# Optimization experiments

Hardware: AMD Instinct MI355X
Metric: run time of the kernel (lower is better)

## Reference

```python
import jax, jax.numpy as jnp
import numpy as np

N_HIDDEN = 32
N_LATENT = 8
FEATS = 128


def _prelu(x, a):
    return jnp.where(x >= 0, x, a * x)


def _gru_cell(x, h, w_ih, w_hh, b_ih, b_hh):
    # PyTorch GRU gate order: r, z, n
    gi = w_ih @ x + b_ih            # (3H,)
    gh = w_hh @ h + b_hh            # (3H,)
    i_r, i_z, i_n = jnp.split(gi, 3)
    h_r, h_z, h_n = jnp.split(gh, 3)
    r = jax.nn.sigmoid(i_r + h_r)
    z = jax.nn.sigmoid(i_z + h_z)
    n = jnp.tanh(i_n + r * h_n)
    return (1.0 - z) * n + z * h


def setup_inputs() -> dict:
    key = jax.random.key(0)
    ks = jax.random.split(key, 32)
    H, L, F = N_HIDDEN, N_LATENT, FEATS
    s = 0.1
    inp = {
        "x": jax.random.normal(ks[0], (F,), dtype=jnp.float32),
        "hidden": jax.random.uniform(ks[1], (2, 1, H), dtype=jnp.float32),
        "eps": jax.random.normal(ks[2], (L,), dtype=jnp.float32),
        # GRU layer 0 (input = feats)
        "w_ih0": jax.random.normal(ks[3], (3 * H, F), dtype=jnp.float32) * s,
        "w_hh0": jax.random.normal(ks[4], (3 * H, H), dtype=jnp.float32) * s,
        "b_ih0": jax.random.normal(ks[5], (3 * H,), dtype=jnp.float32) * s,
        "b_hh0": jax.random.normal(ks[6], (3 * H,), dtype=jnp.float32) * s,
        # GRU layer 1 (input = hidden)
        "w_ih1": jax.random.normal(ks[7], (3 * H, H), dtype=jnp.float32) * s,
        "w_hh1": jax.random.normal(ks[8], (3 * H, H), dtype=jnp.float32) * s,
        "b_ih1": jax.random.normal(ks[9], (3 * H,), dtype=jnp.float32) * s,
        "b_hh1": jax.random.normal(ks[10], (3 * H,), dtype=jnp.float32) * s,
        # encoder
        "enc_w1": jax.random.normal(ks[11], (H, H), dtype=jnp.float32) * s,
        "enc_b1": jax.random.normal(ks[12], (H,), dtype=jnp.float32) * s,
        "enc_a1": jnp.float32(0.25),
        "enc_w2": jax.random.normal(ks[13], (H, H), dtype=jnp.float32) * s,
        "enc_b2": jax.random.normal(ks[14], (H,), dtype=jnp.float32) * s,
        "enc_a2": jnp.float32(0.25),
        "enc_w3": jax.random.normal(ks[15], (2 * L, H), dtype=jnp.float32) * s,
        "enc_b3": jax.random.normal(ks[16], (2 * L,), dtype=jnp.float32) * s,
        # decoder
        "dec_w1": jax.random.normal(ks[17], (H, L), dtype=jnp.float32) * s,
        "dec_b1": jax.random.normal(ks[18], (H,), dtype=jnp.float32) * s,
        "dec_a1": jnp.float32(0.25),
        "dec_w2": jax.random.normal(ks[19], (H, H), dtype=jnp.float32) * s,
        "dec_b2": jax.random.normal(ks[20], (H,), dtype=jnp.float32) * s,
        "dec_a2": jnp.float32(0.25),
        "dec_w3": jax.random.normal(ks[21], (F, H), dtype=jnp.float32) * s,
        "dec_b3": jax.random.normal(ks[22], (F,), dtype=jnp.float32) * s,
    }
    return inp


def reference(x, hidden, eps,
              w_ih0, w_hh0, b_ih0, b_hh0,
              w_ih1, w_hh1, b_ih1, b_hh1,
              enc_w1, enc_b1, enc_a1, enc_w2, enc_b2, enc_a2, enc_w3, enc_b3,
              dec_w1, dec_b1, dec_a1, dec_w2, dec_b2, dec_a2, dec_w3, dec_b3):
    # single timestep, batch 1: treat everything as vectors
    h0 = _gru_cell(x, hidden[0, 0], w_ih0, w_hh0, b_ih0, b_hh0)   # (32,)
    h1 = _gru_cell(h0, hidden[1, 0], w_ih1, w_hh1, b_ih1, b_hh1)  # (32,)
    out = h1  # top-layer GRU output

    e = _prelu(enc_w1 @ out + enc_b1, enc_a1)
    e = _prelu(enc_w2 @ e + enc_b2, enc_a2)
    encoded = enc_w3 @ e + enc_b3                                  # (16,)
    mu, logvar = encoded[:N_LATENT], encoded[N_LATENT:]
    std = jnp.exp(0.5 * logvar)
    z = mu + eps * std

    d = _prelu(dec_w1 @ z + dec_b1, dec_a1)
    d = _prelu(dec_w2 @ d + dec_b2, dec_a2)
    decoded = jax.nn.sigmoid(dec_w3 @ d + dec_b3)                  # (feats,)

    hidden_new = jnp.stack([h0, h1])[:, None, :]                   # (2,1,32)
    return decoded, mu, logvar, hidden_new
```

## Files before the change

kernel.cpp:

```cpp
#include <hip/hip_runtime.h>
#include <math.h>

#define NH 32
#define NL 8
#define NF 128

__device__ __forceinline__ float dot_v4(const float* __restrict__ w,
                                        const float* __restrict__ s, int n4) {
    const float4* w4 = (const float4*)w;
    const float4* s4 = (const float4*)s;
    float acc = 0.f;
#pragma unroll 8
    for (int i = 0; i < n4; ++i) {
        float4 a = w4[i];
        float4 b = s4[i];
        acc = fmaf(a.x, b.x, acc);
        acc = fmaf(a.y, b.y, acc);
        acc = fmaf(a.z, b.z, acc);
        acc = fmaf(a.w, b.w, acc);
    }
    return acc;
}

__device__ __forceinline__ float sigmoidf_(float x) {
    return 1.0f / (1.0f + __expf(-x));
}

__device__ __forceinline__ float preluf_(float x, float a) {
    return x >= 0.0f ? x : a * x;
}

__global__ void __launch_bounds__(128)
omni_anomaly_kernel(const float* __restrict__ x,
                    const float* __restrict__ hidden,
                    const float* __restrict__ eps,
                    const float* __restrict__ w_ih0, const float* __restrict__ w_hh0,
                    const float* __restrict__ b_ih0, const float* __restrict__ b_hh0,
                    const float* __restrict__ w_ih1, const float* __restrict__ w_hh1,
                    const float* __restrict__ b_ih1, const float* __restrict__ b_hh1,
                    const float* __restrict__ enc_w1, const float* __restrict__ enc_b1,
                    const float* __restrict__ enc_a1,
                    const float* __restrict__ enc_w2, const float* __restrict__ enc_b2,
                    const float* __restrict__ enc_a2,
                    const float* __restrict__ enc_w3, const float* __restrict__ enc_b3,
                    const float* __restrict__ dec_w1, const float* __restrict__ dec_b1,
                    const float* __restrict__ dec_a1,
                    const float* __restrict__ dec_w2, const float* __restrict__ dec_b2,
                    const float* __restrict__ dec_a2,
                    const float* __restrict__ dec_w3, const float* __restrict__ dec_b3,
                    float* __restrict__ out) {
    __shared__ __align__(16) float sx[NF];
    __shared__ __align__(16) float sh0[NH];
    __shared__ __align__(16) float sh1[NH];
    __shared__ __align__(16) float gi[3 * NH];
    __shared__ __align__(16) float gh[3 * NH];
    __shared__ __align__(16) float h0n[NH];
    __shared__ __align__(16) float h1n[NH];
    __shared__ __align__(16) float e_buf[NH];
    __shared__ __align__(16) float e2_buf[NH];
    __shared__ __align__(16) float z_buf[NL];
    __shared__ __align__(16) float d1_buf[NH];
    __shared__ __align__(16) float d2_buf[NH];

    const int tid = threadIdx.x;

    if (tid < NF) sx[tid] = x[tid];
    if (tid < NH) {
        sh0[tid] = hidden[tid];
        sh1[tid] = hidden[NH + tid];
    }
    __syncthreads();

    if (tid < 3 * NH) {
        gi[tid] = dot_v4(w_ih0 + tid * NF, sx, NF / 4) + b_ih0[tid];
        gh[tid] = dot_v4(w_hh0 + tid * NH, sh0, NH / 4) + b_hh0[tid];
    }
    __syncthreads();
    if (tid < NH) {
        float r = sigmoidf_(gi[tid] + gh[tid]);
        float z = sigmoidf_(gi[NH + tid] + gh[NH + tid]);
        float n = tanhf(gi[2 * NH + tid] + r * gh[2 * NH + tid]);
        float h = (1.0f - z) * n + z * sh0[tid];
        h0n[tid] = h;
        out[NF + 2 * NL + tid] = h;
    }
    __syncthreads();

    if (tid < 3 * NH) {
        gi[tid] = dot_v4(w_ih1 + tid * NH, h0n, NH / 4) + b_ih1[tid];
        gh[tid] = dot_v4(w_hh1 + tid * NH, sh1, NH / 4) + b_hh1[tid];
    }
    __syncthreads();
    if (tid < NH) {
        float r = sigmoidf_(gi[tid] + gh[tid]);
        float z = sigmoidf_(gi[NH + tid] + gh[NH + tid]);
        float n = tanhf(gi[2 * NH + tid] + r * gh[2 * NH + tid]);
        float h = (1.0f - z) * n + z * sh1[tid];
        h1n[tid] = h;
        out[NF + 2 * NL + NH + tid] = h;
    }
    __syncthreads();

    if (tid < NH) {
        float v = dot_v4(enc_w1 + tid * NH, h1n, NH / 4) + enc_b1[tid];
        e_buf[tid] = preluf_(v, enc_a1[0]);
    }
    __syncthreads();

    if (tid < NH) {
        float v = dot_v4(enc_w2 + tid * NH, e_buf, NH / 4) + enc_b2[tid];
        e2_buf[tid] = preluf_(v, enc_a2[0]);
    }
    __syncthreads();

    if (tid < 2 * NL) {
        float v = dot_v4(enc_w3 + tid * NH, e2_buf, NH / 4) + enc_b3[tid];
        out[NF + tid] = v;
        if (tid < NL) {
            float lv = dot_v4(enc_w3 + (NL + tid) * NH, e2_buf, NH / 4) + enc_b3[NL + tid];
            float std_ = __expf(0.5f * lv);
            z_buf[tid] = v + eps[tid] * std_;
        }
    }
    __syncthreads();

    if (tid < NH) {
        float v = dot_v4(dec_w1 + tid * NL, z_buf, NL / 4) + dec_b1[tid];
        d1_buf[tid] = preluf_(v, dec_a1[0]);
    }
    __syncthreads();

    if (tid < NH) {
        float v = dot_v4(dec_w2 + tid * NH, d1_buf, NH / 4) + dec_b2[tid];
        d2_buf[tid] = preluf_(v, dec_a2[0]);
    }
    __syncthreads();

    if (tid < NF) {
        float v = dot_v4(dec_w3 + tid * NH, d2_buf, NH / 4) + dec_b3[tid];
        out[tid] = sigmoidf_(v);
    }
}

extern "C" void kernel_launch(void* const* d_in, const int* in_sizes, int n_in,
                              void* d_out, int out_size, void* d_ws, size_t ws_size,
                              hipStream_t stream) {
    const float* x      = (const float*)d_in[0];
    const float* hidden = (const float*)d_in[1];
    const float* eps    = (const float*)d_in[2];
    const float* w_ih0  = (const float*)d_in[3];
    const float* w_hh0  = (const float*)d_in[4];
    const float* b_ih0  = (const float*)d_in[5];
    const float* b_hh0  = (const float*)d_in[6];
    const float* w_ih1  = (const float*)d_in[7];
    const float* w_hh1  = (const float*)d_in[8];
    const float* b_ih1  = (const float*)d_in[9];
    const float* b_hh1  = (const float*)d_in[10];
    const float* enc_w1 = (const float*)d_in[11];
    const float* enc_b1 = (const float*)d_in[12];
    const float* enc_a1 = (const float*)d_in[13];
    const float* enc_w2 = (const float*)d_in[14];
    const float* enc_b2 = (const float*)d_in[15];
    const float* enc_a2 = (const float*)d_in[16];
    const float* enc_w3 = (const float*)d_in[17];
    const float* enc_b3 = (const float*)d_in[18];
    const float* dec_w1 = (const float*)d_in[19];
    const float* dec_b1 = (const float*)d_in[20];
    const float* dec_a1 = (const float*)d_in[21];
    const float* dec_w2 = (const float*)d_in[22];
    const float* dec_b2 = (const float*)d_in[23];
    const float* dec_a2 = (const float*)d_in[24];
    const float* dec_w3 = (const float*)d_in[25];
    const float* dec_b3 = (const float*)d_in[26];
    float* out = (float*)d_out;

    omni_anomaly_kernel<<<1, 128, 0, stream>>>(
        x, hidden, eps,
        w_ih0, w_hh0, b_ih0, b_hh0,
        w_ih1, w_hh1, b_ih1, b_hh1,
        enc_w1, enc_b1, enc_a1,
        enc_w2, enc_b2, enc_a2,
        enc_w3, enc_b3,
        dec_w1, dec_b1, dec_a1,
        dec_w2, dec_b2, dec_a2,
        dec_w3, dec_b3,
        out);
}
```

Measured before the change: 11.78 us.

## Run whole network in a single wavefront with wave barriers instead of block syncs

The kernel now launches one 64-thread wavefront and replaces __syncthreads with wave-level barriers, redistributing the GRU and decoder rows so each lane computes several outputs. It also fully unrolls the dot products with four independent accumulators, uses an exp-based tanh, and keeps the previous hidden state in registers. The aim is to cut block-wide barrier cost on a latency-bound serial chain. In exchange each lane does more sequential work, and correctness relies on LDS writes being visible within the wave after a wave barrier.

```diff
diff --git a/kernel.cpp b/kernel.cpp
--- a/kernel.cpp
+++ b/kernel.cpp
@@ -5,32 +5,38 @@
 #define NL 8
 #define NF 128
 
-__device__ __forceinline__ float dot_v4(const float* __restrict__ w,
-                                        const float* __restrict__ s, int n4) {
+#define WSYNC() __builtin_amdgcn_wave_barrier()
+
+template <int N4>
+__device__ __forceinline__ float dotN(const float* __restrict__ w,
+                                      const float* __restrict__ s) {
     const float4* w4 = (const float4*)w;
-    const float4* s4 = (const float4*)s;
-    float acc = 0.f;
-#pragma unroll 8
-    for (int i = 0; i < n4; ++i) {
+    float a0 = 0.f, a1 = 0.f, a2 = 0.f, a3 = 0.f;
+#pragma unroll
+    for (int i = 0; i < N4; ++i) {
         float4 a = w4[i];
-        float4 b = s4[i];
-        acc = fmaf(a.x, b.x, acc);
-        acc = fmaf(a.y, b.y, acc);
-        acc = fmaf(a.z, b.z, acc);
-        acc = fmaf(a.w, b.w, acc);
-    }
-    return acc;
+        a0 = fmaf(a.x, s[4 * i + 0], a0);
+        a1 = fmaf(a.y, s[4 * i + 1], a1);
+        a2 = fmaf(a.z, s[4 * i + 2], a2);
+        a3 = fmaf(a.w, s[4 * i + 3], a3);
+    }
+    return (a0 + a1) + (a2 + a3);
 }
 
 __device__ __forceinline__ float sigmoidf_(float x) {
     return 1.0f / (1.0f + __expf(-x));
 }
 
+__device__ __forceinline__ float tanhf_(float x) {
+    float e = __expf(2.0f * x);
+    return 1.0f - 2.0f / (e + 1.0f);
+}
+
 __device__ __forceinline__ float preluf_(float x, float a) {
     return x >= 0.0f ? x : a * x;
 }
 
-__global__ void __launch_bounds__(128)
+__global__ void __launch_bounds__(64)
 omni_anomaly_kernel(const float* __restrict__ x,
                     const float* __restrict__ hidden,
                     const float* __restrict__ eps,
@@ -52,93 +58,119 @@
     __shared__ __align__(16) float sx[NF];
     __shared__ __align__(16) float sh0[NH];
     __shared__ __align__(16) float sh1[NH];
-    __shared__ __align__(16) float gi[3 * NH];
-    __shared__ __align__(16) float gh[3 * NH];
+    __shared__ __align__(16) float gi0[3 * NH];
+    __shared__ __align__(16) float gh0[3 * NH];
+    __shared__ __align__(16) float gi1[3 * NH];
+    __shared__ __align__(16) float gh1[3 * NH];
     __shared__ __align__(16) float h0n[NH];
     __shared__ __align__(16) float h1n[NH];
-    __shared__ __align__(16) float e_buf[NH];
-    __shared__ __align__(16) float e2_buf[NH];
-    __shared__ __align__(16) float z_buf[NL];
-    __shared__ __align__(16) float d1_buf[NH];
-    __shared__ __align__(16) float d2_buf[NH];
-
-    const int tid = threadIdx.x;
-
-    if (tid < NF) sx[tid] = x[tid];
-    if (tid < NH) {
-        sh0[tid] = hidden[tid];
-        sh1[tid] = hidden[NH + tid];
-    }
-    __syncthreads();
-
-    if (tid < 3 * NH) {
-        gi[tid] = dot_v4(w_ih0 + tid * NF, sx, NF / 4) + b_ih0[tid];
-        gh[tid] = dot_v4(w_hh0 + tid * NH, sh0, NH / 4) + b_hh0[tid];
-    }
-    __syncthreads();
-    if (tid < NH) {
-        float r = sigmoidf_(gi[tid] + gh[tid]);
-        float z = sigmoidf_(gi[NH + tid] + gh[NH + tid]);
-        float n = tanhf(gi[2 * NH + tid] + r * gh[2 * NH + tid]);
-        float h = (1.0f - z) * n + z * sh0[tid];
-        h0n[tid] = h;
-        out[NF + 2 * NL + tid] = h;
-    }
-    __syncthreads();
-
-    if (tid < 3 * NH) {
-        gi[tid] = dot_v4(w_ih1 + tid * NH, h0n, NH / 4) + b_ih1[tid];
-        gh[tid] = dot_v4(w_hh1 + tid * NH, sh1, NH / 4) + b_hh1[tid];
-    }
-    __syncthreads();
-    if (tid < NH) {
-        float r = sigmoidf_(gi[tid] + gh[tid]);
-        float z = sigmoidf_(gi[NH + tid] + gh[NH + tid]);
-        float n = tanhf(gi[2 * NH + tid] + r * gh[2 * NH + tid]);
-        float h = (1.0f - z) * n + z * sh1[tid];
-        h1n[tid] = h;
-        out[NF + 2 * NL + NH + tid] = h;
-    }
-    __syncthreads();
-
-    if (tid < NH) {
-        float v = dot_v4(enc_w1 + tid * NH, h1n, NH / 4) + enc_b1[tid];
-        e_buf[tid] = preluf_(v, enc_a1[0]);
-    }
-    __syncthreads();
-
-    if (tid < NH) {
-        float v = dot_v4(enc_w2 + tid * NH, e_buf, NH / 4) + enc_b2[tid];
-        e2_buf[tid] = preluf_(v, enc_a2[0]);
-    }
-    __syncthreads();
-
-    if (tid < 2 * NL) {
-        float v = dot_v4(enc_w3 + tid * NH, e2_buf, NH / 4) + enc_b3[tid];
-        out[NF + tid] = v;
-        if (tid < NL) {
-            float lv = dot_v4(enc_w3 + (NL + tid) * NH, e2_buf, NH / 4) + enc_b3[NL + tid];
-            float std_ = __expf(0.5f * lv);
-            z_buf[tid] = v + eps[tid] * std_;
+    __shared__ __align__(16) float e1b[NH];
+    __shared__ __align__(16) float e2b[NH];
+    __shared__ __align__(16) float eo[2 * NL];
+    __shared__ __align__(16) float zb[NL];
+    __shared__ __align__(16) float d1b[NH];
+    __shared__ __align__(16) float d2b[NH];
+
+    const int t = threadIdx.x;
+
+    float h0reg = 0.f, h1reg = 0.f;
+    if (t < NF / 4) {
+        ((float4*)sx)[t] = ((const float4*)x)[t];
+    }
+    if (t < NH) {
+        h0reg = hidden[t];
+        h1reg = hidden[NH + t];
+        sh0[t] = h0reg;
+        sh1[t] = h1reg;
+    }
+    WSYNC();
+
+    gi0[t] = dotN<NF / 4>(w_ih0 + t * NF, sx) + b_ih0[t];
+    if (t < 32) {
+        int r = 64 + t;
+        gi0[r] = dotN<NF / 4>(w_ih0 + r * NF, sx) + b_ih0[r];
+    } else {
+        int r = 3 * (t - 32);
+        gh0[r + 0] = dotN<NH / 4>(w_hh0 + (r + 0) * NH, sh0) + b_hh0[r + 0];
+        gh0[r + 1] = dotN<NH / 4>(w_hh0 + (r + 1) * NH, sh0) + b_hh0[r + 1];
+        gh0[r + 2] = dotN<NH / 4>(w_hh0 + (r + 2) * NH, sh0) + b_hh0[r + 2];
+    }
+    WSYNC();
+
+    if (t < NH) {
+        float r = sigmoidf_(gi0[t] + gh0[t]);
+        float z = sigmoidf_(gi0[NH + t] + gh0[NH + t]);
+        float n = tanhf_(gi0[2 * NH + t] + r * gh0[2 * NH + t]);
+        float h = (1.0f - z) * n + z * h0reg;
+        h0n[t] = h;
+        out[NF + 2 * NL + t] = h;
+    }
+    WSYNC();
+
+#pragma unroll
+    for (int k = 0; k < 3; ++k) {
+        int d = t + 64 * k;
+        if (d < 3 * NH) {
+            gi1[d] = dotN<NH / 4>(w_ih1 + d * NH, h0n) + b_ih1[d];
+        } else {
+            int r = d - 3 * NH;
+            gh1[r] = dotN<NH / 4>(w_hh1 + r * NH, sh1) + b_hh1[r];
         }
     }
-    __syncthreads();
-
-    if (tid < NH) {
-        float v = dot_v4(dec_w1 + tid * NL, z_buf, NL / 4) + dec_b1[tid];
-        d1_buf[tid] = preluf_(v, dec_a1[0]);
-    }
-    __syncthreads();
-
-    if (tid < NH) {
-        float v = dot_v4(dec_w2 + tid * NH, d1_buf, NH / 4) + dec_b2[tid];
-        d2_buf[tid] = preluf_(v, dec_a2[0]);
-    }
-    __syncthreads();
-
-    if (tid < NF) {
-        float v = dot_v4(dec_w3 + tid * NH, d2_buf, NH / 4) + dec_b3[tid];
-        out[tid] = sigmoidf_(v);
+    WSYNC();
+
+    if (t < NH) {
+        float r = sigmoidf_(gi1[t] + gh1[t]);
+        float z = sigmoidf_(gi1[NH + t] + gh1[NH + t]);
+        float n = tanhf_(gi1[2 * NH + t] + r * gh1[2 * NH + t]);
+        float h = (1.0f - z) * n + z * h1reg;
+        h1n[t] = h;
+        out[NF + 2 * NL + NH + t] = h;
+    }
+    WSYNC();
+
+    if (t < NH) {
+        float v = dotN<NH / 4>(enc_w1 + t * NH, h1n) + enc_b1[t];
+        e1b[t] = preluf_(v, enc_a1[0]);
+    }
+    WSYNC();
+
+    if (t < NH) {
+        float v = dotN<NH / 4>(enc_w2 + t * NH, e1b) + enc_b2[t];
+        e2b[t] = preluf_(v, enc_a2[0]);
+    }
+    WSYNC();
+
+    if (t < 2 * NL) {
+        float v = dotN<NH / 4>(enc_w3 + t * NH, e2b) + enc_b3[t];
+        eo[t] = v;
+        out[NF + t] = v;
+    }
+    WSYNC();
+
+    if (t < NL) {
+        zb[t] = eo[t] + eps[t] * __expf(0.5f * eo[NL + t]);
+    }
+    WSYNC();
+
+    if (t < NH) {
+        float v = dotN<NL / 4>(dec_w1 + t * NL, zb) + dec_b1[t];
+        d1b[t] = preluf_(v, dec_a1[0]);
+    }
+    WSYNC();
+
+    if (t < NH) {
+        float v = dotN<NH / 4>(dec_w2 + t * NH, d1b) + dec_b2[t];
+        d2b[t] = preluf_(v, dec_a2[0]);
+    }
+    WSYNC();
+
+    {
+        float v0 = dotN<NH / 4>(dec_w3 + t * NH, d2b) + dec_b3[t];
+        out[t] = sigmoidf_(v0);
+        int r = 64 + t;
+        float v1 = dotN<NH / 4>(dec_w3 + r * NH, d2b) + dec_b3[r];
+        out[r] = sigmoidf_(v1);
     }
 }
 
@@ -174,7 +206,7 @@
     const float* dec_b3 = (const float*)d_in[26];
     float* out = (float*)d_out;
 
-    omni_anomaly_kernel<<<1, 128, 0, stream>>>(
+    omni_anomaly_kernel<<<1, 64, 0, stream>>>(
         x, hidden, eps,
         w_ih0, w_hh0, b_ih0, b_hh0,
         w_ih1, w_hh1, b_ih1, b_hh1,
```

Measured after the change: 12.85 us. 9.0% more time.
